# Kernel tuning notes

Measured on AMD Instinct MI355X. Metric: run time of the kernel, lower is better.

The kernel has to match this reference:

```python
import jax, jax.numpy as jnp
import numpy as np

V, H, L, B = 50257, 1024, 10, 256

def setup_inputs() -> dict:
    key = jax.random.key(0)
    ks = jax.random.split(key, 16)
    s = 0.02
    return {
        "tokens": jax.random.randint(ks[0], (1, B), 0, V),
        "hidden": jax.random.normal(ks[1], (1, B, H), jnp.float32),
        "encoder_outputs": jax.random.normal(ks[2], (L, H), jnp.float32),
        "emb": jax.random.normal(ks[3], (V, H), jnp.float32) * s,
        "attn_W": jax.random.normal(ks[4], (L, 2 * H), jnp.float32) * s,
        "attn_b": jnp.zeros((L,), jnp.float32),
        "comb_W": jax.random.normal(ks[5], (H, 2 * H), jnp.float32) * s,
        "comb_b": jnp.zeros((H,), jnp.float32),
        "W_ih": jax.random.normal(ks[6], (3 * H, H), jnp.float32) * s,
        "W_hh": jax.random.normal(ks[7], (3 * H, H), jnp.float32) * s,
        "b_ih": jnp.zeros((3 * H,), jnp.float32),
        "b_hh": jnp.zeros((3 * H,), jnp.float32),
        "out_W": jax.random.normal(ks[8], (V, H), jnp.float32) * s,
        "out_b": jnp.zeros((V,), jnp.float32),
    }

def reference(tokens, hidden, encoder_outputs, emb, attn_W, attn_b, comb_W, comb_b,
              W_ih, W_hh, b_ih, b_hh, out_W, out_b):
    # Embedding lookup (dropout = identity, eval mode)
    embedded = emb[tokens[0]]            # [B, H]
    h = hidden[-1]                       # [B, H]
    # Attention over encoder outputs
    attn_logits = jnp.concatenate([embedded, h], axis=1) @ attn_W.T + attn_b
    attn_weights = jax.nn.softmax(attn_logits, axis=1)          # [B, L]
    attn_applied = attn_weights @ encoder_outputs                # [B, H]
    # Combine + relu -> GRU input
    x = jnp.concatenate([embedded, attn_applied], axis=1) @ comb_W.T + comb_b
    x = jax.nn.relu(x)                   # [B, H]
    # Single GRU step (PyTorch gate ordering: r, z, n)
    gi = x @ W_ih.T + b_ih               # [B, 3H]
    gh = h @ W_hh.T + b_hh               # [B, 3H]
    i_r, i_z, i_n = jnp.split(gi, 3, axis=1)
    h_r, h_z, h_n = jnp.split(gh, 3, axis=1)
    r = jax.nn.sigmoid(i_r + h_r)
    z = jax.nn.sigmoid(i_z + h_z)
    n = jnp.tanh(i_n + r * h_n)
    h_new = (1.0 - z) * n + z * h        # [B, H]
    # Output projection + log_softmax
    output = jax.nn.log_softmax(h_new @ out_W.T + out_b, axis=1)  # [B, V]
    return (output, h_new[None], attn_weights)
```

## Files before the change

### kernel.cpp

```cpp
#include <hip/hip_runtime.h>
#include <hip/hip_bf16.h>
#include <math.h>
#include <stdint.h>

#define B_SZ 256
#define H_SZ 1024
#define L_SZ 10
#define V_SZ 50257

typedef __attribute__((ext_vector_type(8))) short short8;
typedef __attribute__((ext_vector_type(4))) float floatx4;

__device__ __forceinline__ unsigned f2bf_bits(float f) {
    unsigned u = __float_as_uint(f);
    return (u + 0x7FFFu + ((u >> 16) & 1u)) >> 16;
}

__device__ __forceinline__ short8 cvt8(float4 a, float4 b) {
    unsigned r0, r1, r2, r3;
    asm("v_cvt_pk_bf16_f32 %0, %1, %2" : "=v"(r0) : "v"(a.x), "v"(a.y));
    asm("v_cvt_pk_bf16_f32 %0, %1, %2" : "=v"(r1) : "v"(a.z), "v"(a.w));
    asm("v_cvt_pk_bf16_f32 %0, %1, %2" : "=v"(r2) : "v"(b.x), "v"(b.y));
    asm("v_cvt_pk_bf16_f32 %0, %1, %2" : "=v"(r3) : "v"(b.z), "v"(b.w));
    union { unsigned u[4]; short8 s; } u;
    u.u[0] = r0; u.u[1] = r1; u.u[2] = r2; u.u[3] = r3;
    return u.s;
}

#define WSTRIDE 40

template<int MSUB, int RELU, int PF, int ABF>
__device__ __forceinline__ void gemm_body(
    short (*lwb)[64 * WSTRIDE],
    const void* __restrict__ A, const float* __restrict__ W,
    const float* __restrict__ bias, float* __restrict__ C,
    int N, int K)
{
    const int tid  = threadIdx.x;
    const int wave = tid >> 6;
    const int lane = tid & 63;
    const int quad = lane >> 4;
    const int l16  = lane & 15;

    const int n0 = blockIdx.x * 64;
    const int m_base = blockIdx.y * (MSUB * 64) + wave * (MSUB * 16);

    const int wr = tid >> 2;
    const int wc = (tid & 3) * 8;
    int wrow = n0 + wr;
    if (wrow >= N) wrow = N - 1;
    const float* wp = W + (size_t)wrow * K + wc;

    const int nc = K >> 5;

    const float* af[MSUB];
    const short* ab[MSUB];
#pragma unroll
    for (int ms = 0; ms < MSUB; ++ms) {
        int m = m_base + ms * 16 + l16;
        if (ABF) ab[ms] = (const short*)A + (size_t)m * K + quad * 8;
        else     af[ms] = (const float*)A + (size_t)m * K + quad * 8;
    }

    floatx4 zero = {0.f, 0.f, 0.f, 0.f};
    floatx4 acc[MSUB][4];
#pragma unroll
    for (int ms = 0; ms < MSUB; ++ms)
#pragma unroll
        for (int ns = 0; ns < 4; ++ns) acc[ms][ns] = zero;

    float4 wreg[PF][2];
#pragma unroll
    for (int p = 0; p < PF; ++p) {
        wreg[p][0] = *(const float4*)(wp + p * 32);
        wreg[p][1] = *(const float4*)(wp + p * 32 + 4);
    }
    *(short8*)&lwb[0][wr * WSTRIDE + wc] = cvt8(wreg[0][0], wreg[0][1]);
    asm volatile("s_waitcnt lgkmcnt(0)" ::: "memory");
    __builtin_amdgcn_s_barrier();

    for (int c0 = 0; c0 < nc; c0 += PF) {
#pragma unroll
        for (int p = 0; p < PF; ++p) {
            const int c   = c0 + p;
            const int buf = p & 1;

            if (c + PF < nc) {
                wreg[p][0] = *(const float4*)(wp + (c + PF) * 32);
                wreg[p][1] = *(const float4*)(wp + (c + PF) * 32 + 4);
            }

            short8 bfrag[4];
#pragma unroll
            for (int ns = 0; ns < 4; ++ns)
                bfrag[ns] = *(const short8*)&lwb[buf][(ns * 16 + l16) * WSTRIDE + quad * 8];
#pragma unroll
            for (int ms = 0; ms < MSUB; ++ms) {
                short8 afrag;
                if (ABF) {
                    afrag = *(const short8*)(ab[ms] + c * 32);
                } else {
                    float4 a0 = *(const float4*)(af[ms] + c * 32);
                    float4 a1 = *(const float4*)(af[ms] + c * 32 + 4);
                    afrag = cvt8(a0, a1);
                }
#pragma unroll
                for (int ns = 0; ns < 4; ++ns)
                    acc[ms][ns] = __builtin_amdgcn_mfma_f32_16x16x32_bf16(
                        afrag, bfrag[ns], acc[ms][ns], 0, 0, 0);
            }

            if (c + 1 < nc) {
                const int q = (p + 1 == PF) ? 0 : p + 1;
                *(short8*)&lwb[buf ^ 1][wr * WSTRIDE + wc] =
                    cvt8(wreg[q][0], wreg[q][1]);
            }

            asm volatile("s_waitcnt lgkmcnt(0)" ::: "memory");
            __builtin_amdgcn_s_barrier();
        }
    }

    float bia[4];
#pragma unroll
    for (int ns = 0; ns < 4; ++ns) {
        int n = n0 + ns * 16 + l16;
        bia[ns] = (n < N) ? bias[n] : 0.f;
    }
#pragma unroll
    for (int ms = 0; ms < MSUB; ++ms) {
        int mb = m_base + ms * 16 + quad * 4;
#pragma unroll
        for (int ns = 0; ns < 4; ++ns) {
            int n = n0 + ns * 16 + l16;
            if (n < N) {
#pragma unroll
                for (int i = 0; i < 4; ++i) {
                    float v = acc[ms][ns][i] + bia[ns];
                    if (RELU) v = fmaxf(v, 0.f);
                    C[(size_t)(mb + i) * N + n] = v;
                }
            }
        }
    }
}

template<int MSUB, int RELU, int PF, int ABF>
__global__ __launch_bounds__(256) void gemm_mfma(
    const void* __restrict__ A, const float* __restrict__ W,
    const float* __restrict__ bias, float* __restrict__ C,
    int N, int K)
{
    __shared__ __align__(16) short lwb[2][64 * WSTRIDE];
    gemm_body<MSUB, RELU, PF, ABF>(lwb, A, W, bias, C, N, K);
}

template<int MSUB, int RELU, int PF>
__global__ __launch_bounds__(256) void gemm_dual(
    const void* __restrict__ A0, const float* __restrict__ W0,
    const float* __restrict__ b0, float* __restrict__ C0,
    const void* __restrict__ A1, const float* __restrict__ W1,
    const float* __restrict__ b1, float* __restrict__ C1,
    int N, int K)
{
    __shared__ __align__(16) short lwb[2][64 * WSTRIDE];
    const void*  A = blockIdx.z ? A1 : A0;
    const float* W = blockIdx.z ? W1 : W0;
    const float* b = blockIdx.z ? b1 : b0;
    float*       C = blockIdx.z ? C1 : C0;
    gemm_body<MSUB, RELU, PF, 0>(lwb, A, W, b, C, N, K);
}

__global__ __launch_bounds__(256) void attn_kernel(
    const int* __restrict__ tokens, const float* __restrict__ hidden,
    const float* __restrict__ enc, const float* __restrict__ emb,
    const float* __restrict__ attn_W, const float* __restrict__ attn_b,
    float* __restrict__ cat_out, float* __restrict__ attn_w_out)
{
    const int b = blockIdx.x;
    const int tid = threadIdx.x;
    const int tok = tokens[b];
    const float* erow = emb + (size_t)tok * H_SZ;
    const float* hrow = hidden + (size_t)b * H_SZ;

    __shared__ float red[L_SZ][256];
    __shared__ float wts[L_SZ];

    float acc[L_SZ];
#pragma unroll
    for (int l = 0; l < L_SZ; ++l) acc[l] = 0.f;

    for (int i = tid; i < H_SZ; i += 256) {
        float e = erow[i];
        float hv = hrow[i];
        cat_out[(size_t)b * 2 * H_SZ + i] = e;
#pragma unroll
        for (int l = 0; l < L_SZ; ++l) {
            acc[l] += e * attn_W[l * 2 * H_SZ + i] + hv * attn_W[l * 2 * H_SZ + H_SZ + i];
        }
    }
#pragma unroll
    for (int l = 0; l < L_SZ; ++l) red[l][tid] = acc[l];
    __syncthreads();
    for (int s = 128; s > 0; s >>= 1) {
        if (tid < s) {
#pragma unroll
            for (int l = 0; l < L_SZ; ++l) red[l][tid] += red[l][tid + s];
        }
        __syncthreads();
    }
    if (tid == 0) {
        float m = -INFINITY;
        float lg[L_SZ];
#pragma unroll
        for (int l = 0; l < L_SZ; ++l) {
            lg[l] = red[l][0] + attn_b[l];
            m = fmaxf(m, lg[l]);
        }
        float s = 0.f;
#pragma unroll
        for (int l = 0; l < L_SZ; ++l) {
            float e = expf(lg[l] - m);
            wts[l] = e;
            s += e;
        }
        float inv = 1.f / s;
#pragma unroll
        for (int l = 0; l < L_SZ; ++l) {
            wts[l] *= inv;
            attn_w_out[(size_t)b * L_SZ + l] = wts[l];
        }
    }
    __syncthreads();

    for (int i = tid; i < H_SZ; i += 256) {
        float s = 0.f;
#pragma unroll
        for (int l = 0; l < L_SZ; ++l) s += wts[l] * enc[l * H_SZ + i];
        cat_out[(size_t)b * 2 * H_SZ + H_SZ + i] = s;
    }
}

__global__ __launch_bounds__(256) void gru_combine(
    const float* __restrict__ gi, const float* __restrict__ gh,
    const float* __restrict__ hidden, float* __restrict__ h_new,
    short* __restrict__ hb16)
{
    int idx = blockIdx.x * blockDim.x + threadIdx.x;
    if (idx >= B_SZ * H_SZ) return;
    int b = idx >> 10;
    int j = idx & (H_SZ - 1);
    const float* gib = gi + (size_t)b * 3 * H_SZ;
    const float* ghb = gh + (size_t)b * 3 * H_SZ;
    float i_r = gib[j], i_z = gib[H_SZ + j], i_n = gib[2 * H_SZ + j];
    float h_r = ghb[j], h_z = ghb[H_SZ + j], h_n = ghb[2 * H_SZ + j];
    float r = 1.f / (1.f + expf(-(i_r + h_r)));
    float z = 1.f / (1.f + expf(-(i_z + h_z)));
    float n = tanhf(i_n + r * h_n);
    float h = hidden[idx];
    float hn = (1.f - z) * n + z * h;
    h_new[idx] = hn;
    if (hb16) hb16[idx] = (short)f2bf_bits(hn);
}

__global__ __launch_bounds__(1024) void logsoftmax_v2(float* __restrict__ out)
{
    const int b = blockIdx.x;
    float* row = out + (size_t)b * V_SZ;
    const int tid = threadIdx.x;
    const int wave = tid >> 6;
    const int lane = tid & 63;

    const int head = (int)(((16u - ((uintptr_t)row & 15u)) & 15u) >> 2);
    const int nv = (V_SZ - head) >> 2;
    const float4* r4 = (const float4*)(row + head);
    const int tail_start = head + (nv << 2);

    float m = -INFINITY, s = 0.f;
    if (tid < head) {
        float v = row[tid];
        m = v; s = 1.f;
    }
    for (int i = tid; i < nv; i += 1024) {
        float4 v = r4[i];
        float mv = fmaxf(fmaxf(v.x, v.y), fmaxf(v.z, v.w));
        if (mv > m) { s *= expf(m - mv); m = mv; }
        s += expf(v.x - m) + expf(v.y - m) + expf(v.z - m) + expf(v.w - m);
    }
    for (int i = tail_start + tid; i < V_SZ; i += 1024) {
        float v = row[i];
        if (v > m) { s *= expf(m - v); m = v; }
        s += expf(v - m);
    }

    for (int off = 32; off > 0; off >>= 1) {
        float m2 = __shfl_down(m, off);
        float s2 = __shfl_down(s, off);
        float mn = fmaxf(m, m2);
        s = s * expf(m - mn) + s2 * expf(m2 - mn);
        m = mn;
    }
    __shared__ float smax[16], ssum[16], slse;
    if (lane == 0) { smax[wave] = m; ssum[wave] = s; }
    __syncthreads();
    if (tid == 0) {
        float M = smax[0], S = ssum[0];
        for (int w = 1; w < 16; ++w) {
            float mn = fmaxf(M, smax[w]);
            S = S * expf(M - mn) + ssum[w] * expf(smax[w] - mn);
            M = mn;
        }
        slse = M + logf(S);
    }
    __syncthreads();
    const float lse = slse;

    if (tid < head) row[tid] -= lse;
    float4* w4 = (float4*)(row + head);
    for (int i = tid; i < nv; i += 1024) {
        float4 v = r4[i];
        v.x -= lse; v.y -= lse; v.z -= lse; v.w -= lse;
        w4[i] = v;
    }
    for (int i = tail_start + tid; i < V_SZ; i += 1024) row[i] -= lse;
}

extern "C" void kernel_launch(void* const* d_in, const int* in_sizes, int n_in,
                              void* d_out, int out_size, void* d_ws, size_t ws_size,
                              hipStream_t stream)
{
    const int*   tokens = (const int*)d_in[0];
    const float* hidden = (const float*)d_in[1];
    const float* enc    = (const float*)d_in[2];
    const float* emb    = (const float*)d_in[3];
    const float* attn_W = (const float*)d_in[4];
    const float* attn_b = (const float*)d_in[5];
    const float* comb_W = (const float*)d_in[6];
    const float* comb_b = (const float*)d_in[7];
    const float* W_ih   = (const float*)d_in[8];
    const float* W_hh   = (const float*)d_in[9];
    const float* b_ih   = (const float*)d_in[10];
    const float* b_hh   = (const float*)d_in[11];
    const float* out_W  = (const float*)d_in[12];
    const float* out_b  = (const float*)d_in[13];

    float* out = (float*)d_out;
    float* logits     = out;
    float* h_new      = out + (size_t)B_SZ * V_SZ;
    float* attn_w_out = h_new + (size_t)B_SZ * H_SZ;

    const size_t need = (size_t)B_SZ * H_SZ * 9 * sizeof(float)
                      + (size_t)B_SZ * H_SZ * sizeof(short);
    const bool use_ws = (d_ws != nullptr) && (ws_size >= need);

    float* scratch = use_ws ? (float*)d_ws : logits;
    float* cat = scratch;
    float* x   = cat + (size_t)B_SZ * 2 * H_SZ;
    float* gi  = x   + (size_t)B_SZ * H_SZ;
    float* gh  = gi  + (size_t)B_SZ * 3 * H_SZ;
    short* hb16 = use_ws ? (short*)(gh + (size_t)B_SZ * 3 * H_SZ) : nullptr;

    attn_kernel<<<B_SZ, 256, 0, stream>>>(tokens, hidden, enc, emb, attn_W, attn_b,
                                          cat, attn_w_out);
    gemm_mfma<1, 1, 4, 0><<<dim3(H_SZ / 64, 4), 256, 0, stream>>>(
        cat, comb_W, comb_b, x, H_SZ, 2 * H_SZ);
    gemm_dual<1, 0, 4><<<dim3(3 * H_SZ / 64, 4, 2), 256, 0, stream>>>(
        x, W_ih, b_ih, gi,
        hidden, W_hh, b_hh, gh, 3 * H_SZ, H_SZ);
    gru_combine<<<(B_SZ * H_SZ + 255) / 256, 256, 0, stream>>>(gi, gh, hidden,
                                                               h_new, hb16);
    if (use_ws)
        gemm_mfma<4, 0, 2, 1><<<dim3((V_SZ + 63) / 64, 1), 256, 0, stream>>>(
            (const void*)hb16, out_W, out_b, logits, V_SZ, H_SZ);
    else
        gemm_mfma<4, 0, 2, 0><<<dim3((V_SZ + 63) / 64, 1), 256, 0, stream>>>(
            (const void*)h_new, out_W, out_b, logits, V_SZ, H_SZ);
    logsoftmax_v2<<<B_SZ, 1024, 0, stream>>>(logits);
}
```

Baseline: 621.9 us.

## Stream GEMM tiles via async global-to-LDS loads with multi-stage pipeline and bf16 activations

Replaces the register-staged, double-buffered weight path in the MFMA GEMM with direct global_load_lds copies into a DEPTH-stage ring buffer in shared memory. Both the weight tiles and the activation tiles now come through LDS, using XOR-swizzled offsets, with vmcnt-based waits. The small GEMMs now take bf16 activations, produced directly by the attention kernel and the combine GEMM epilogue, which halves activation traffic. The aim is to hide global latency on the large vocab projection and the GRU GEMMs, at the cost of more LDS, which may lower occupancy, and fragile hand-tuned waitcnt counts.

After: 584.0 us. -6.1%, faster.

```diff
diff --git a/kernel.cpp b/kernel.cpp
--- a/kernel.cpp
+++ b/kernel.cpp
@@ -1,5 +1,4 @@
 #include <hip/hip_runtime.h>
-#include <hip/hip_bf16.h>
 #include <math.h>
 #include <stdint.h>
 
@@ -27,15 +26,35 @@
     return u.s;
 }
 
-#define WSTRIDE 40
-
-template<int MSUB, int RELU, int PF, int ABF>
+__device__ __forceinline__ void glds16(const void* g, void* l) {
+    __builtin_amdgcn_global_load_lds(
+        (const __attribute__((address_space(1))) void*)g,
+        (__attribute__((address_space(3))) void*)l, 16, 0, 0);
+}
+
+template<int N> __device__ __forceinline__ void waitvm() {
+    if constexpr (N == 0)       asm volatile("s_waitcnt vmcnt(0)" ::: "memory");
+    else if constexpr (N == 3)  asm volatile("s_waitcnt vmcnt(3)" ::: "memory");
+    else if constexpr (N == 4)  asm volatile("s_waitcnt vmcnt(4)" ::: "memory");
+    else if constexpr (N == 6)  asm volatile("s_waitcnt vmcnt(6)" ::: "memory");
+    else if constexpr (N == 8)  asm volatile("s_waitcnt vmcnt(8)" ::: "memory");
+    else if constexpr (N == 9)  asm volatile("s_waitcnt vmcnt(9)" ::: "memory");
+    else if constexpr (N == 10) asm volatile("s_waitcnt vmcnt(10)" ::: "memory");
+    else if constexpr (N == 12) asm volatile("s_waitcnt vmcnt(12)" ::: "memory");
+    else if constexpr (N == 20) asm volatile("s_waitcnt vmcnt(20)" ::: "memory");
+    else static_assert(N == 0, "unsupported vmcnt literal");
+}
+
+template<int MSUB, int RELU, int DEPTH, int ABF>
 __device__ __forceinline__ void gemm_body(
-    short (*lwb)[64 * WSTRIDE],
+    float* wbuf, short* abufS, float* abufF,
     const void* __restrict__ A, const float* __restrict__ W,
-    const float* __restrict__ bias, float* __restrict__ C,
-    int N, int K)
-{
+    const float* __restrict__ bias, float* __restrict__ Cf,
+    short* __restrict__ C16, int N, int K)
+{
+    constexpr int AOPS = ABF ? MSUB : 2 * MSUB;
+    constexpr int OPS  = 2 + AOPS;
+
     const int tid  = threadIdx.x;
     const int wave = tid >> 6;
     const int lane = tid & 63;
@@ -44,22 +63,53 @@
 
     const int n0 = blockIdx.x * 64;
     const int m_base = blockIdx.y * (MSUB * 64) + wave * (MSUB * 16);
-
-    const int wr = tid >> 2;
-    const int wc = (tid & 3) * 8;
-    int wrow = n0 + wr;
-    if (wrow >= N) wrow = N - 1;
-    const float* wp = W + (size_t)wrow * K + wc;
-
     const int nc = K >> 5;
 
-    const float* af[MSUB];
-    const short* ab[MSUB];
+    const float* wsrc[2];
+#pragma unroll
+    for (int i = 0; i < 2; ++i) {
+        int row = n0 + 8 * (2 * wave + i) + (lane >> 3);
+        if (row >= N) row = N - 1;
+        wsrc[i] = W + (size_t)row * K + (((lane & 7) ^ (lane >> 3)) << 2);
+    }
+    const short* asrcS[ABF ? MSUB : 1];
+    const float* asrcF[ABF ? 1 : 2 * MSUB];
+    if constexpr (ABF) {
+#pragma unroll
+        for (int j = 0; j < MSUB; ++j) {
+            int row = m_base + 16 * j + (lane >> 2);
+            asrcS[j] = (const short*)A + (size_t)row * K
+                     + (((lane & 3) ^ ((lane >> 3) & 3)) << 3);
+        }
+    } else {
+#pragma unroll
+        for (int j = 0; j < 2 * MSUB; ++j) {
+            int row = m_base + 8 * j + (lane >> 3);
+            asrcF[j] = (const float*)A + (size_t)row * K
+                     + (((lane & 7) ^ (lane >> 3)) << 2);
+        }
+    }
+
+    int boff[4][2];
+#pragma unroll
+    for (int ns = 0; ns < 4; ++ns) {
+        int R = ns * 16 + l16;
+#pragma unroll
+        for (int h = 0; h < 2; ++h)
+            boff[ns][h] = R * 128 + (((2 * quad + h) ^ (l16 & 7)) << 4);
+    }
+    int aoff[MSUB][2];
 #pragma unroll
     for (int ms = 0; ms < MSUB; ++ms) {
-        int m = m_base + ms * 16 + l16;
-        if (ABF) ab[ms] = (const short*)A + (size_t)m * K + quad * 8;
-        else     af[ms] = (const float*)A + (size_t)m * K + quad * 8;
+        int Rl = wave * MSUB * 16 + ms * 16 + l16;
+        if constexpr (ABF) {
+            aoff[ms][0] = Rl * 64 + ((quad ^ ((l16 >> 1) & 3)) << 4);
+            aoff[ms][1] = 0;
+        } else {
+#pragma unroll
+            for (int h = 0; h < 2; ++h)
+                aoff[ms][h] = Rl * 128 + (((2 * quad + h) ^ (l16 & 7)) << 4);
+        }
     }
 
     floatx4 zero = {0.f, 0.f, 0.f, 0.f};
@@ -69,56 +119,75 @@
 #pragma unroll
         for (int ns = 0; ns < 4; ++ns) acc[ms][ns] = zero;
 
-    float4 wreg[PF][2];
-#pragma unroll
-    for (int p = 0; p < PF; ++p) {
-        wreg[p][0] = *(const float4*)(wp + p * 32);
-        wreg[p][1] = *(const float4*)(wp + p * 32 + 4);
-    }
-    *(short8*)&lwb[0][wr * WSTRIDE + wc] = cvt8(wreg[0][0], wreg[0][1]);
-    asm volatile("s_waitcnt lgkmcnt(0)" ::: "memory");
-    __builtin_amdgcn_s_barrier();
-
-    for (int c0 = 0; c0 < nc; c0 += PF) {
-#pragma unroll
-        for (int p = 0; p < PF; ++p) {
-            const int c   = c0 + p;
-            const int buf = p & 1;
-
-            if (c + PF < nc) {
-                wreg[p][0] = *(const float4*)(wp + (c + PF) * 32);
-                wreg[p][1] = *(const float4*)(wp + (c + PF) * 32 + 4);
+    auto issue = [&](int slot) {
+#pragma unroll
+        for (int i = 0; i < 2; ++i) {
+            glds16(wsrc[i], (char*)wbuf + slot * 8192 + (2 * wave + i) * 1024);
+            wsrc[i] += 32;
+        }
+        if constexpr (ABF) {
+#pragma unroll
+            for (int j = 0; j < MSUB; ++j) {
+                glds16(asrcS[j], (char*)abufS + slot * (MSUB * 4096)
+                                 + (wave * MSUB + j) * 1024);
+                asrcS[j] += 32;
             }
-
-            short8 bfrag[4];
+        } else {
+#pragma unroll
+            for (int j = 0; j < 2 * MSUB; ++j) {
+                glds16(asrcF[j], (char*)abufF + slot * (MSUB * 8192)
+                                 + (wave * 2 * MSUB + j) * 1024);
+                asrcF[j] += 32;
+            }
+        }
+    };
+
+#pragma unroll
+    for (int d = 0; d < DEPTH; ++d) issue(d);
+
+    int slot = 0;
+    for (int c = 0; c < nc; ++c) {
+        const int rem = nc - 1 - c;
+        if (rem >= DEPTH - 1)  waitvm<OPS * (DEPTH - 1)>();
+        else if (rem == 2)     waitvm<((DEPTH >= 4) ? 2 * OPS : 0)>();
+        else if (rem == 1)     waitvm<((DEPTH >= 3) ? OPS : 0)>();
+        else                   waitvm<0>();
+        asm volatile("s_barrier" ::: "memory");
+
+        const char* wb = (const char*)wbuf + slot * 8192;
+        short8 bfr[4];
+#pragma unroll
+        for (int ns = 0; ns < 4; ++ns) {
+            float4 x0 = *(const float4*)(wb + boff[ns][0]);
+            float4 x1 = *(const float4*)(wb + boff[ns][1]);
+            bfr[ns] = cvt8(x0, x1);
+        }
+        short8 afr[MSUB];
+        if constexpr (ABF) {
+            const char* ab = (const char*)abufS + slot * (MSUB * 4096);
+#pragma unroll
+            for (int ms = 0; ms < MSUB; ++ms)
+                afr[ms] = *(const short8*)(ab + aoff[ms][0]);
+        } else {
+            const char* ab = (const char*)abufF + slot * (MSUB * 8192);
+#pragma unroll
+            for (int ms = 0; ms < MSUB; ++ms) {
+                float4 a0 = *(const float4*)(ab + aoff[ms][0]);
+                float4 a1 = *(const float4*)(ab + aoff[ms][1]);
+                afr[ms] = cvt8(a0, a1);
+            }
+        }
+#pragma unroll
+        for (int ms = 0; ms < MSUB; ++ms)
 #pragma unroll
             for (int ns = 0; ns < 4; ++ns)
-                bfrag[ns] = *(const short8*)&lwb[buf][(ns * 16 + l16) * WSTRIDE + quad * 8];
-#pragma unroll
-            for (int ms = 0; ms < MSUB; ++ms) {
-                short8 afrag;
-                if (ABF) {
-                    afrag = *(const short8*)(ab[ms] + c * 32);
-                } else {
-                    float4 a0 = *(const float4*)(af[ms] + c * 32);
-                    float4 a1 = *(const float4*)(af[ms] + c * 32 + 4);
-                    afrag = cvt8(a0, a1);
-                }
-#pragma unroll
-                for (int ns = 0; ns < 4; ++ns)
-                    acc[ms][ns] = __builtin_amdgcn_mfma_f32_16x16x32_bf16(
-                        afrag, bfrag[ns], acc[ms][ns], 0, 0, 0);
-            }
-
-            if (c + 1 < nc) {
-                const int q = (p + 1 == PF) ? 0 : p + 1;
-                *(short8*)&lwb[buf ^ 1][wr * WSTRIDE + wc] =
-                    cvt8(wreg[q][0], wreg[q][1]);
-            }
-
-            asm volatile("s_waitcnt lgkmcnt(0)" ::: "memory");
-            __builtin_amdgcn_s_barrier();
-        }
+                acc[ms][ns] = __builtin_amdgcn_mfma_f32_16x16x32_bf16(
+                    afr[ms], bfr[ns], acc[ms][ns], 0, 0, 0);
+
+        asm volatile("s_waitcnt lgkmcnt(0)" ::: "memory");
+        asm volatile("s_barrier" ::: "memory");
+        if (c + DEPTH < nc) issue(slot);
+        if (++slot == DEPTH) slot = 0;
     }
 
     float bia[4];
@@ -138,24 +207,27 @@
                 for (int i = 0; i < 4; ++i) {
                     float v = acc[ms][ns][i] + bia[ns];
                     if (RELU) v = fmaxf(v, 0.f);
-                    C[(size_t)(mb + i) * N + n] = v;
+                    if (Cf)  Cf[(size_t)(mb + i) * N + n] = v;
+                    if (C16) C16[(size_t)(mb + i) * N + n] = (short)f2bf_bits(v);
                 }
             }
         }
     }
 }
 
-template<int MSUB, int RELU, int PF, int ABF>
-__global__ __launch_bounds__(256) void gemm_mfma(
+template<int MSUB, int RELU, int DEPTH, int ABF>
+__global__ __launch_bounds__(256) void gemm_k(
     const void* __restrict__ A, const float* __restrict__ W,
-    const float* __restrict__ bias, float* __restrict__ C,
-    int N, int K)
-{
-    __shared__ __align__(16) short lwb[2][64 * WSTRIDE];
-    gemm_body<MSUB, RELU, PF, ABF>(lwb, A, W, bias, C, N, K);
-}
-
-template<int MSUB, int RELU, int PF>
+    const float* __restrict__ bias, float* __restrict__ Cf,
+    short* __restrict__ C16, int N, int K)
+{
+    __shared__ __align__(16) float wbuf[DEPTH * 64 * 32];
+    __shared__ __align__(16) short abufS[ABF ? DEPTH * MSUB * 2048 : 8];
+    __shared__ __align__(16) float abufF[ABF ? 8 : DEPTH * MSUB * 2048];
+    gemm_body<MSUB, RELU, DEPTH, ABF>(wbuf, abufS, abufF, A, W, bias, Cf, C16, N, K);
+}
+
+template<int MSUB, int RELU, int DEPTH, int ABF>
 __global__ __launch_bounds__(256) void gemm_dual(
     const void* __restrict__ A0, const float* __restrict__ W0,
     const float* __restrict__ b0, float* __restrict__ C0,
@@ -163,19 +235,22 @@
     const float* __restrict__ b1, float* __restrict__ C1,
     int N, int K)
 {
-    __shared__ __align__(16) short lwb[2][64 * WSTRIDE];
+    __shared__ __align__(16) float wbuf[DEPTH * 64 * 32];
+    __shared__ __align__(16) short abufS[ABF ? DEPTH * MSUB * 2048 : 8];
+    __shared__ __align__(16) float abufF[ABF ? 8 : DEPTH * MSUB * 2048];
     const void*  A = blockIdx.z ? A1 : A0;
     const float* W = blockIdx.z ? W1 : W0;
     const float* b = blockIdx.z ? b1 : b0;
     float*       C = blockIdx.z ? C1 : C0;
-    gemm_body<MSUB, RELU, PF, 0>(lwb, A, W, b, C, N, K);
+    gemm_body<MSUB, RELU, DEPTH, ABF>(wbuf, abufS, abufF, A, W, b, C, nullptr, N, K);
 }
 
 __global__ __launch_bounds__(256) void attn_kernel(
     const int* __restrict__ tokens, const float* __restrict__ hidden,
     const float* __restrict__ enc, const float* __restrict__ emb,
     const float* __restrict__ attn_W, const float* __restrict__ attn_b,
-    float* __restrict__ cat_out, float* __restrict__ attn_w_out)
+    float* __restrict__ catf, short* __restrict__ cat16,
+    short* __restrict__ h16, float* __restrict__ attn_w_out)
 {
     const int b = blockIdx.x;
     const int tid = threadIdx.x;
@@ -193,7 +268,9 @@
     for (int i = tid; i < H_SZ; i += 256) {
         float e = erow[i];
         float hv = hrow[i];
-        cat_out[(size_t)b * 2 * H_SZ + i] = e;
+        if (catf)  catf[(size_t)b * 2 * H_SZ + i] = e;
+        if (cat16) cat16[(size_t)b * 2 * H_SZ + i] = (short)f2bf_bits(e);
+        if (h16)   h16[(size_t)b * H_SZ + i] = (short)f2bf_bits(hv);
 #pragma unroll
         for (int l = 0; l < L_SZ; ++l) {
             acc[l] += e * attn_W[l * 2 * H_SZ + i] + hv * attn_W[l * 2 * H_SZ + H_SZ + i];
@@ -237,7 +314,8 @@
         float s = 0.f;
 #pragma unroll
         for (int l = 0; l < L_SZ; ++l) s += wts[l] * enc[l * H_SZ + i];
-        cat_out[(size_t)b * 2 * H_SZ + H_SZ + i] = s;
+        if (catf)  catf[(size_t)b * 2 * H_SZ + H_SZ + i] = s;
+        if (cat16) cat16[(size_t)b * 2 * H_SZ + H_SZ + i] = (short)f2bf_bits(s);
     }
 }
 
@@ -349,31 +427,46 @@
     float* h_new      = out + (size_t)B_SZ * V_SZ;
     float* attn_w_out = h_new + (size_t)B_SZ * H_SZ;
 
-    const size_t need = (size_t)B_SZ * H_SZ * 9 * sizeof(float)
-                      + (size_t)B_SZ * H_SZ * sizeof(short);
+    const size_t need = (size_t)B_SZ * 5 * H_SZ * sizeof(short)
+                      + (size_t)B_SZ * 6 * H_SZ * sizeof(float);
     const bool use_ws = (d_ws != nullptr) && (ws_size >= need);
 
-    float* scratch = use_ws ? (float*)d_ws : logits;
-    float* cat = scratch;
-    float* x   = cat + (size_t)B_SZ * 2 * H_SZ;
-    float* gi  = x   + (size_t)B_SZ * H_SZ;
-    float* gh  = gi  + (size_t)B_SZ * 3 * H_SZ;
-    short* hb16 = use_ws ? (short*)(gh + (size_t)B_SZ * 3 * H_SZ) : nullptr;
-
-    attn_kernel<<<B_SZ, 256, 0, stream>>>(tokens, hidden, enc, emb, attn_W, attn_b,
-                                          cat, attn_w_out);
-    gemm_mfma<1, 1, 4, 0><<<dim3(H_SZ / 64, 4), 256, 0, stream>>>(
-        cat, comb_W, comb_b, x, H_SZ, 2 * H_SZ);
-    gemm_dual<1, 0, 4><<<dim3(3 * H_SZ / 64, 4, 2), 256, 0, stream>>>(
-        x, W_ih, b_ih, gi,
-        hidden, W_hh, b_hh, gh, 3 * H_SZ, H_SZ);
-    gru_combine<<<(B_SZ * H_SZ + 255) / 256, 256, 0, stream>>>(gi, gh, hidden,
-                                                               h_new, hb16);
-    if (use_ws)
-        gemm_mfma<4, 0, 2, 1><<<dim3((V_SZ + 63) / 64, 1), 256, 0, stream>>>(
-            (const void*)hb16, out_W, out_b, logits, V_SZ, H_SZ);
-    else
-        gemm_mfma<4, 0, 2, 0><<<dim3((V_SZ + 63) / 64, 1), 256, 0, stream>>>(
-            (const void*)h_new, out_W, out_b, logits, V_SZ, H_SZ);
+    if (use_ws) {
+        short* cat16 = (short*)d_ws;
+        short* x16   = cat16 + (size_t)B_SZ * 2 * H_SZ;
+        short* hin16 = x16   + (size_t)B_SZ * H_SZ;
+        short* hb16  = hin16 + (size_t)B_SZ * H_SZ;
+        float* gi    = (float*)(hb16 + (size_t)B_SZ * H_SZ);
+        float* gh    = gi + (size_t)B_SZ * 3 * H_SZ;
+
+        attn_kernel<<<B_SZ, 256, 0, stream>>>(tokens, hidden, enc, emb, attn_W,
+                                              attn_b, nullptr, cat16, hin16,
+                                              attn_w_out);
+        gemm_k<1, 1, 4, 1><<<dim3(H_SZ / 64, 4), 256, 0, stream>>>(
+            cat16, comb_W, comb_b, nullptr, x16, H_SZ, 2 * H_SZ);
+        gemm_dual<1, 0, 4, 1><<<dim3(3 * H_SZ / 64, 4, 2), 256, 0, stream>>>(
+            x16, W_ih, b_ih, gi, hin16, W_hh, b_hh, gh, 3 * H_SZ, H_SZ);
+        gru_combine<<<(B_SZ * H_SZ + 255) / 256, 256, 0, stream>>>(
+            gi, gh, hidden, h_new, hb16);
+        gemm_k<4, 0, 3, 1><<<dim3((V_SZ + 63) / 64, 1), 256, 0, stream>>>(
+            hb16, out_W, out_b, logits, nullptr, V_SZ, H_SZ);
+    } else {
+        float* cat = logits;
+        float* x   = cat + (size_t)B_SZ * 2 * H_SZ;
+        float* gi  = x   + (size_t)B_SZ * H_SZ;
+        float* gh  = gi  + (size_t)B_SZ * 3 * H_SZ;
+
+        attn_kernel<<<B_SZ, 256, 0, stream>>>(tokens, hidden, enc, emb, attn_W,
+                                              attn_b, cat, nullptr, nullptr,
+                                              attn_w_out);
+        gemm_k<1, 1, 3, 0><<<dim3(H_SZ / 64, 4), 256, 0, stream>>>(
+            cat, comb_W, comb_b, x, nullptr, H_SZ, 2 * H_SZ);
+        gemm_dual<1, 0, 3, 0><<<dim3(3 * H_SZ / 64, 4, 2), 256, 0, stream>>>(
+            x, W_ih, b_ih, gi, hidden, W_hh, b_hh, gh, 3 * H_SZ, H_SZ);
+        gru_combine<<<(B_SZ * H_SZ + 255) / 256, 256, 0, stream>>>(
+            gi, gh, hidden, h_new, nullptr);
+        gemm_k<4, 0, 2, 0><<<dim3((V_SZ + 63) / 64, 1), 256, 0, stream>>>(
+            h_new, out_W, out_b, logits, nullptr, V_SZ, H_SZ);
+    }
     logsoftmax_v2<<<B_SZ, 1024, 0, stream>>>(logits);
 }
```
